# Kernel tuning notes

Measured on AMD Instinct MI355X. Metric: run time of the kernel, lower is better.

Reference implementation:

```python
import jax, jax.numpy as jnp
import numpy as np

B, S, H, N = 8, 64, 256, 256  # batch, max_seq_length, hidden_size, num_neurons


def setup_inputs() -> dict:
    key = jax.random.key(0)
    k1, k2 = jax.random.split(key)
    return {
        "inputs": jax.random.normal(k1, (B, S, H), dtype=jnp.float32),
        "threshes": jax.random.uniform(k2, (N,), dtype=jnp.float32),
        "accumulations": jnp.zeros((N,), dtype=jnp.float32),
        "data_type": 1,  # 1 = 'positive', 0 = 'negative'
    }


def reference(inputs, threshes, accumulations, data_type):
    x = jax.nn.sigmoid(inputs)                       # [B,S,H]
    B_, S_, H_ = x.shape
    N_ = threshes.shape[0]
    # the torch double loop iterates i over seq then j over hidden -> flatten to T = S*H steps
    xt = x.reshape(B_, S_ * H_).T                    # [T,B]

    def step(state, xb):
        # torch detaches the carried accumulator every step
        acc = jax.lax.stop_gradient(state)[None, :] + xb[:, None]   # [B,N]
        spike = acc > threshes                                       # [B,N] bool
        out = jnp.where(spike, acc, jnp.zeros((), acc.dtype))        # spike * acc
        new_state = jnp.max(acc - out, axis=0)                       # max over batch -> [N]
        return new_state, (out, spike)

    _, (outs, spikes) = jax.lax.scan(step, accumulations, xt)        # [T,B,N]
    # stack over j at dim=2 then i at dim=1 -> [B,S,N,H]
    outs = outs.reshape(S_, H_, B_, N_).transpose(2, 0, 3, 1)
    spikes = spikes.reshape(S_, H_, B_, N_).transpose(2, 0, 3, 1)
    outputs = jax.nn.sigmoid(outs)                                   # [B,S,N,H]

    # goodness: L2 norm over neuron dim (axis=2), scaled
    norm = jnp.linalg.norm(outputs, axis=2) / outputs.shape[2]       # [B,S,H]
    goodness = jnp.sum(norm) / (B_ * S_ * outputs.shape[3])
    loss = -goodness if data_type == 1 else goodness
    return outputs, spikes, loss
```

## Files before the change

### kernel.cpp

```cpp
#include <hip/hip_runtime.h>
#include <math.h>

#define BB 8
#define SS 64
#define HH 256
#define NNEUR 256
#define TT (SS*HH)
#define CL 128
#define NC (TT/CL)
#define OUT1 ((size_t)BB*SS*NNEUR*HH)

__device__ __forceinline__ float sigf(float v) {
    return 1.0f / (1.0f + expf(-v));
}

__device__ __forceinline__ float lif_step(float s, const float* __restrict__ x8, float thr) {
    float best = 0.0f;
#pragma unroll
    for (int b = 0; b < BB; ++b) {
        float acc = s + x8[b];
        float cand = (acc > thr) ? 0.0f : acc;
        best = fmaxf(best, cand);
    }
    return best;
}

__device__ __forceinline__ void load_x8(const float* __restrict__ xT, int t, float* x8) {
    const float4* xp = (const float4*)(xT + (size_t)t * 8);
    float4 xa = xp[0], xb = xp[1];
    x8[0]=xa.x; x8[1]=xa.y; x8[2]=xa.z; x8[3]=xa.w;
    x8[4]=xb.x; x8[5]=xb.y; x8[6]=xb.z; x8[7]=xb.w;
}

__global__ void __launch_bounds__(256) k_prep(const float* __restrict__ in, float* __restrict__ xT,
                                              float* __restrict__ gacc) {
    int t = blockIdx.x * 256 + threadIdx.x;
    if (t == 0) *gacc = 0.0f;
    float v[BB];
#pragma unroll
    for (int b = 0; b < BB; ++b) v[b] = sigf(in[(size_t)b*TT + t]);
    float4* o = (float4*)(xT + (size_t)t * 8);
    o[0] = make_float4(v[0], v[1], v[2], v[3]);
    o[1] = make_float4(v[4], v[5], v[6], v[7]);
}

__global__ void __launch_bounds__(256) k_spec(const float* __restrict__ xT,
                                              const float* __restrict__ threshes,
                                              const float* __restrict__ acc0,
                                              const float* __restrict__ guess,
                                              float* __restrict__ states,
                                              float* __restrict__ chunkFinal) {
    const int n = threadIdx.x;
    const int c = blockIdx.x;
    const float thr = threshes[n];
    float s;
    if (c == 0)      s = acc0[n];
    else if (guess)  s = guess[(size_t)(c-1)*NNEUR + n];
    else             s = 0.0f;

    __shared__ float buf[NNEUR][33];
    const int tbase = c * CL;

    if (states) {
        for (int t0 = 0; t0 < CL; t0 += 32) {
            for (int tt = 0; tt < 32; ++tt) {
                const int t = tbase + t0 + tt;
                buf[n][tt] = s;
                float x8[8];
                load_x8(xT, t, x8);
                s = lif_step(s, x8, thr);
            }
            __syncthreads();
#pragma unroll
            for (int i = 0; i < 32; ++i) {
                int r  = i*8 + (threadIdx.x >> 5);
                int cc = threadIdx.x & 31;
                states[(size_t)r*TT + tbase + t0 + cc] = buf[r][cc];
            }
            __syncthreads();
        }
    } else {
        for (int tt = 0; tt < CL; ++tt) {
            float x8[8];
            load_x8(xT, tbase + tt, x8);
            s = lif_step(s, x8, thr);
        }
    }
    chunkFinal[(size_t)c*NNEUR + n] = s;
}

__global__ void __launch_bounds__(64) k_fixup(const float* __restrict__ xT,
                                              const float* __restrict__ threshes,
                                              const float* __restrict__ acc0,
                                              const float* __restrict__ finalA,
                                              const float* __restrict__ finalB,
                                              float* __restrict__ states) {
    const int n = blockIdx.x * 64 + threadIdx.x;
    const float thr = threshes[n];
    float s = acc0[n];
    for (int c = 0; c < NC; ++c) {
        float used = (c == 0) ? acc0[n] : finalA[(size_t)(c-1)*NNEUR + n];
        float finB = finalB[(size_t)c*NNEUR + n];
        bool need = (s != used);
        if (__any(need)) {
            const int tbase = c * CL;
            for (int tt = 0; tt < CL; ++tt) {
                const int t = tbase + tt;
                float stored = states[(size_t)n*TT + t];
                if (need && s == stored) need = false;
                if (!__any(need)) break;
                if (need) states[(size_t)n*TT + t] = s;
                float x8[8];
                load_x8(xT, t, x8);
                float sn = lif_step(s, x8, thr);
                if (need) s = sn;
            }
        }
        s = need ? s : finB;
    }
}

__global__ void __launch_bounds__(256) k_out(const float* __restrict__ in,
                                             const float* __restrict__ threshes,
                                             const float* __restrict__ states,
                                             float* __restrict__ out,
                                             float* __restrict__ gacc) {
    const int h  = threadIdx.x;
    const int s_ = blockIdx.x >> 3;
    const int b  = blockIdx.x & 7;
    const int t  = s_ * HH + h;
    const float xv = sigf(in[(size_t)b*TT + t]);
    __shared__ float thrs[NNEUR];
    thrs[h] = threshes[h];
    __syncthreads();

    float* outputs = out;
    float* spikes  = out + OUT1;
    float lossAcc = 0.0f;
    size_t base = ((size_t)(b*SS + s_) * NNEUR) * HH + h;
    for (int n = 0; n < NNEUR; ++n) {
        float st  = states[(size_t)n*TT + t];
        float acc = st + xv;
        bool spike = acc > thrs[n];
        float o = spike ? sigf(acc) : 0.5f;
        outputs[base + (size_t)n*HH] = o;
        spikes [base + (size_t)n*HH] = spike ? 1.0f : 0.0f;
        lossAcc = fmaf(o, o, lossAcc);
    }
    float v = sqrtf(lossAcc) * (1.0f / (256.0f * 131072.0f));
    for (int off = 32; off > 0; off >>= 1) v += __shfl_down(v, off);
    __shared__ float wsum[4];
    if ((threadIdx.x & 63) == 0) wsum[threadIdx.x >> 6] = v;
    __syncthreads();
    if (threadIdx.x == 0) atomicAdd(gacc, wsum[0] + wsum[1] + wsum[2] + wsum[3]);
}

__global__ void k_final(const float* __restrict__ gacc, const int* __restrict__ dtype,
                        float* __restrict__ lossOut) {
    float g = *gacc;
    *lossOut = (dtype[0] == 1) ? -g : g;
}

extern "C" void kernel_launch(void* const* d_in, const int* in_sizes, int n_in,
                              void* d_out, int out_size, void* d_ws, size_t ws_size,
                              hipStream_t stream) {
    const float* in       = (const float*)d_in[0];
    const float* threshes = (const float*)d_in[1];
    const float* acc0     = (const float*)d_in[2];
    const int*   dtype    = (const int*)d_in[3];
    float* out = (float*)d_out;

    char* ws = (char*)d_ws;
    float* xT     = (float*)(ws);
    float* states = (float*)(ws + 524288);
    float* finalA = (float*)(ws + 524288 + 16777216);
    float* finalB = (float*)(ws + 524288 + 16777216 + 131072);
    float* gacc   = (float*)(ws + 524288 + 16777216 + 262144);

    k_prep <<<TT/256, 256, 0, stream>>>(in, xT, gacc);
    k_spec <<<NC, 256, 0, stream>>>(xT, threshes, acc0, nullptr, nullptr, finalA);
    k_spec <<<NC, 256, 0, stream>>>(xT, threshes, acc0, finalA, states, finalB);
    k_fixup<<<NNEUR/64, 64, 0, stream>>>(xT, threshes, acc0, finalA, finalB, states);
    k_out  <<<BB*SS, 256, 0, stream>>>(in, threshes, states, out, gacc);
    k_final<<<1, 1, 0, stream>>>(gacc, dtype, out + 2*OUT1);
}
```

Before: 210.0 us.

## Fuse final loss kernel via ticket, prefetch fixup finals, nontemporal output stores

Removes the single-thread final kernel by having the last finishing block of the output kernel write the loss, using an atomic ticket counter. The fixup loop now prefetches the next chunk's speculative-state values one iteration ahead. The output kernel uses nontemporal stores for the large outputs and spikes arrays, a fast exp intrinsic, and unroll-by-4 on the neuron loop. These target launch overhead, load latency in the serial fixup, and cache pollution from the write-dominated output. The fast exp trades a little accuracy for speed.

Result: no change. 206.1 us (-1.8%).

```diff
diff --git a/kernel.cpp b/kernel.cpp
--- a/kernel.cpp
+++ b/kernel.cpp
@@ -9,6 +9,7 @@
 #define CL 128
 #define NC (TT/CL)
 #define OUT1 ((size_t)BB*SS*NNEUR*HH)
+#define NBLK_OUT (BB*SS)
 
 __device__ __forceinline__ float sigf(float v) {
     return 1.0f / (1.0f + expf(-v));
@@ -33,9 +34,9 @@
 }
 
 __global__ void __launch_bounds__(256) k_prep(const float* __restrict__ in, float* __restrict__ xT,
-                                              float* __restrict__ gacc) {
+                                              float* __restrict__ gacc, unsigned* __restrict__ ticket) {
     int t = blockIdx.x * 256 + threadIdx.x;
-    if (t == 0) *gacc = 0.0f;
+    if (t == 0) { *gacc = 0.0f; *ticket = 0u; }
     float v[BB];
 #pragma unroll
     for (int b = 0; b < BB; ++b) v[b] = sigf(in[(size_t)b*TT + t]);
@@ -98,9 +99,15 @@
     const int n = blockIdx.x * 64 + threadIdx.x;
     const float thr = threshes[n];
     float s = acc0[n];
+    float used_next = acc0[n];
+    float finB_next = finalB[n];
     for (int c = 0; c < NC; ++c) {
-        float used = (c == 0) ? acc0[n] : finalA[(size_t)(c-1)*NNEUR + n];
-        float finB = finalB[(size_t)c*NNEUR + n];
+        float used = used_next;
+        float finB = finB_next;
+        if (c + 1 < NC) {
+            used_next = finalA[(size_t)c*NNEUR + n];
+            finB_next = finalB[(size_t)(c+1)*NNEUR + n];
+        }
         bool need = (s != used);
         if (__any(need)) {
             const int tbase = c * CL;
@@ -124,7 +131,9 @@
                                              const float* __restrict__ threshes,
                                              const float* __restrict__ states,
                                              float* __restrict__ out,
-                                             float* __restrict__ gacc) {
+                                             float* __restrict__ gacc,
+                                             unsigned* __restrict__ ticket,
+                                             const int* __restrict__ dtype) {
     const int h  = threadIdx.x;
     const int s_ = blockIdx.x >> 3;
     const int b  = blockIdx.x & 7;
@@ -138,13 +147,14 @@
     float* spikes  = out + OUT1;
     float lossAcc = 0.0f;
     size_t base = ((size_t)(b*SS + s_) * NNEUR) * HH + h;
+#pragma unroll 4
     for (int n = 0; n < NNEUR; ++n) {
         float st  = states[(size_t)n*TT + t];
         float acc = st + xv;
         bool spike = acc > thrs[n];
-        float o = spike ? sigf(acc) : 0.5f;
-        outputs[base + (size_t)n*HH] = o;
-        spikes [base + (size_t)n*HH] = spike ? 1.0f : 0.0f;
+        float o = spike ? (1.0f / (1.0f + __expf(-acc))) : 0.5f;
+        __builtin_nontemporal_store(o, &outputs[base + (size_t)n*HH]);
+        __builtin_nontemporal_store(spike ? 1.0f : 0.0f, &spikes[base + (size_t)n*HH]);
         lossAcc = fmaf(o, o, lossAcc);
     }
     float v = sqrtf(lossAcc) * (1.0f / (256.0f * 131072.0f));
@@ -152,13 +162,16 @@
     __shared__ float wsum[4];
     if ((threadIdx.x & 63) == 0) wsum[threadIdx.x >> 6] = v;
     __syncthreads();
-    if (threadIdx.x == 0) atomicAdd(gacc, wsum[0] + wsum[1] + wsum[2] + wsum[3]);
-}
-
-__global__ void k_final(const float* __restrict__ gacc, const int* __restrict__ dtype,
-                        float* __restrict__ lossOut) {
-    float g = *gacc;
-    *lossOut = (dtype[0] == 1) ? -g : g;
+    if (threadIdx.x == 0) {
+        atomicAdd(gacc, wsum[0] + wsum[1] + wsum[2] + wsum[3]);
+        __threadfence();
+        unsigned old = atomicAdd(ticket, 1u);
+        if (old == NBLK_OUT - 1) {
+            __threadfence();
+            float g = *(volatile float*)gacc;
+            out[2*OUT1] = (dtype[0] == 1) ? -g : g;
+        }
+    }
 }
 
 extern "C" void kernel_launch(void* const* d_in, const int* in_sizes, int n_in,
@@ -171,16 +184,16 @@
     float* out = (float*)d_out;
 
     char* ws = (char*)d_ws;
-    float* xT     = (float*)(ws);
-    float* states = (float*)(ws + 524288);
-    float* finalA = (float*)(ws + 524288 + 16777216);
-    float* finalB = (float*)(ws + 524288 + 16777216 + 131072);
-    float* gacc   = (float*)(ws + 524288 + 16777216 + 262144);
+    float*    xT     = (float*)(ws);
+    float*    states = (float*)(ws + 524288);
+    float*    finalA = (float*)(ws + 524288 + 16777216);
+    float*    finalB = (float*)(ws + 524288 + 16777216 + 131072);
+    float*    gacc   = (float*)(ws + 524288 + 16777216 + 262144);
+    unsigned* ticket = (unsigned*)(ws + 524288 + 16777216 + 262144 + 4);
 
-    k_prep <<<TT/256, 256, 0, stream>>>(in, xT, gacc);
+    k_prep <<<TT/256, 256, 0, stream>>>(in, xT, gacc, ticket);
     k_spec <<<NC, 256, 0, stream>>>(xT, threshes, acc0, nullptr, nullptr, finalA);
     k_spec <<<NC, 256, 0, stream>>>(xT, threshes, acc0, finalA, states, finalB);
     k_fixup<<<NNEUR/64, 64, 0, stream>>>(xT, threshes, acc0, finalA, finalB, states);
-    k_out  <<<BB*SS, 256, 0, stream>>>(in, threshes, states, out, gacc);
-    k_final<<<1, 1, 0, stream>>>(gacc, dtype, out + 2*OUT1);
+    k_out  <<<NBLK_OUT, 256, 0, stream>>>(in, threshes, states, out, gacc, ticket, dtype);
 }
```
